# Optimization experiments

Hardware: AMD Instinct MI355X
Metric: run time of the kernel (lower is better)

The kernel has to match this reference:

```python
import jax, jax.numpy as jnp
import numpy as np

NUM_HEADS = 4
LN_EPS = 1e-5


def setup_inputs() -> dict:
    key = jax.random.key(0)
    ks = jax.random.split(key, 5)
    C = 256
    x = jax.random.normal(ks[0], (2, C, 64, 64), dtype=jnp.float32)
    in_proj_w = jax.random.normal(ks[1], (3 * C, C), dtype=jnp.float32) * (1.0 / np.sqrt(C))
    in_proj_b = jax.random.normal(ks[2], (3 * C,), dtype=jnp.float32) * 0.02
    out_w = jax.random.normal(ks[3], (C, C), dtype=jnp.float32) * (1.0 / np.sqrt(C))
    out_b = jax.random.normal(ks[4], (C,), dtype=jnp.float32) * 0.02
    ln_g = jnp.ones((C,), dtype=jnp.float32)
    ln_b = jnp.zeros((C,), dtype=jnp.float32)
    return {"x": x, "in_proj_w": in_proj_w, "in_proj_b": in_proj_b,
            "out_w": out_w, "out_b": out_b, "ln_g": ln_g, "ln_b": ln_b}


def reference(x, in_proj_w, in_proj_b, out_w, out_b, ln_g, ln_b):
    b, c, H, W = x.shape
    S = H * W  # 4096 == max_tokens -> no pooling, no interpolation
    hd = c // NUM_HEADS
    t = x.reshape(b, c, S).transpose(0, 2, 1)  # (b, S, c)
    # fused QKV projection (in_proj_weight is [3c, c], rows = q,k,v blocks)
    qkv = t @ in_proj_w.T + in_proj_b  # (b, S, 3c)
    q, k, v = jnp.split(qkv, 3, axis=-1)
    def to_heads(a):
        return a.reshape(b, S, NUM_HEADS, hd).transpose(0, 2, 1, 3)  # (b, h, S, d)
    q = to_heads(q) * (1.0 / np.sqrt(hd))
    k = to_heads(k)
    v = to_heads(v)
    scores = jnp.einsum('bhqd,bhkd->bhqk', q, k)      # (b, h, S, S)
    probs = jax.nn.softmax(scores, axis=-1)
    attn = jnp.einsum('bhqk,bhkd->bhqd', probs, v)    # (b, h, S, d)
    attn = attn.transpose(0, 2, 1, 3).reshape(b, S, c)
    out = attn @ out_w.T + out_b                      # output projection
    # LayerNorm over channel dim
    mu = jnp.mean(out, axis=-1, keepdims=True)
    var = jnp.mean(jnp.square(out - mu), axis=-1, keepdims=True)
    out = (out - mu) * jax.lax.rsqrt(var + LN_EPS) * ln_g + ln_b
    return out.transpose(0, 2, 1).reshape(b, c, H, W)
```

## Files before the change

kernel.cpp:

```cpp
#include <hip/hip_runtime.h>
#include <cstddef>

#define S_TOK 4096
#define CDIM 256
#define NHEADS 4
#define HDIM 64
#define LSK 72
#define LDA 36
#define LDY 264
#define LOG2E 1.44269504f

typedef __attribute__((ext_vector_type(8))) short short8;
typedef __attribute__((ext_vector_type(4))) float floatx4;

__device__ inline unsigned short f2bf(float f) {
  union { float f; unsigned u; } v;
  v.f = f;
  unsigned r = v.u + 0x7fff + ((v.u >> 16) & 1);
  return (unsigned short)(r >> 16);
}
__device__ inline float bf2f(unsigned short u) {
  union { unsigned u; float f; } v;
  v.u = ((unsigned)u) << 16;
  return v.f;
}
__device__ inline unsigned pack_bf16(float a, float b) {
#if __has_builtin(__builtin_amdgcn_cvt_pk_bf16_f32)
  typedef __bf16 bf16x2 __attribute__((ext_vector_type(2)));
  union { bf16x2 v; unsigned u; } r;
  r.v = __builtin_amdgcn_cvt_pk_bf16_f32(a, b);
  return r.u;
#else
  return ((unsigned)f2bf(b) << 16) | f2bf(a);
#endif
}

__global__ __launch_bounds__(256) void prep_kernel(
    const float* __restrict__ x, const float* __restrict__ ipw,
    const float* __restrict__ ow, unsigned short* __restrict__ wbf,
    unsigned short* __restrict__ owbf, unsigned short* __restrict__ xbfT) {
  __shared__ __align__(16) unsigned short T[64 * 72];
  const int tid = threadIdx.x;
  if (blockIdx.x < 256) {
    int idx = blockIdx.x * 256 + tid;
    float4 f;
    unsigned short* dst;
    if (idx < 49152) {
      f = ((const float4*)ipw)[idx];
      dst = wbf + idx * 4;
    } else {
      int j = idx - 49152;
      f = ((const float4*)ow)[j];
      dst = owbf + j * 4;
    }
    ushort4 u;
    u.x = f2bf(f.x); u.y = f2bf(f.y); u.z = f2bf(f.z); u.w = f2bf(f.w);
    *(ushort4*)dst = u;
    return;
  }
  const int bid = blockIdx.x - 256;
  const int s0 = (bid & 63) * 64, c0 = ((bid >> 6) & 3) * 64, b = bid >> 8;
  const int c_l = tid >> 2, q4 = tid & 3;
  const float4* src = (const float4*)(x + (((size_t)(b * CDIM + c0 + c_l)) << 12) + s0);
#pragma unroll
  for (int i = 0; i < 4; ++i) {
    int chunk = i * 4 + q4;
    float4 f = src[chunk];
    T[(chunk * 4 + 0) * 72 + c_l] = f2bf(f.x);
    T[(chunk * 4 + 1) * 72 + c_l] = f2bf(f.y);
    T[(chunk * 4 + 2) * 72 + c_l] = f2bf(f.z);
    T[(chunk * 4 + 3) * 72 + c_l] = f2bf(f.w);
  }
  __syncthreads();
  const int s_l = tid >> 2;
  unsigned short* drow = xbfT + ((size_t)((b << 12) + s0 + s_l)) * CDIM + c0;
#pragma unroll
  for (int i = 0; i < 2; ++i) {
    int chunk = i * 4 + q4;
    uint4 u = *(const uint4*)&T[s_l * 72 + chunk * 8];
    *(uint4*)(drow + chunk * 8) = u;
  }
}

__global__ __launch_bounds__(256) void qkv_gemm_kernel(
    const unsigned short* __restrict__ xbfT, const unsigned short* __restrict__ wbf,
    const float* __restrict__ ipb, unsigned short* __restrict__ q16,
    unsigned short* __restrict__ k16, unsigned short* __restrict__ vt16) {
  __shared__ __align__(16) unsigned short As[128 * LDA];
  __shared__ __align__(16) unsigned short Bs[64 * LDA];
  const int tid = threadIdx.x;
  const int wave = tid >> 6, lane = tid & 63;
  const int quad = lane >> 4, l16 = lane & 15;
  const int n0 = blockIdx.x * 64;
  const int tok0 = blockIdx.y * 128;
  const int b = blockIdx.z;

  const int r1 = tid >> 2, c1 = tid & 3;
  const unsigned short* gA = xbfT + ((size_t)(b * S_TOK + tok0 + r1)) * CDIM + c1 * 8;
  const unsigned short* gB = wbf + ((size_t)(n0 + r1)) * CDIM + c1 * 8;
  unsigned short* wA = &As[r1 * LDA + c1 * 8];
  unsigned short* wB = &Bs[r1 * LDA + c1 * 8];

  floatx4 acc[2][4];
#pragma unroll
  for (int mt = 0; mt < 2; ++mt)
#pragma unroll
    for (int nt = 0; nt < 4; ++nt) acc[mt][nt] = (floatx4){0.f, 0.f, 0.f, 0.f};

  uint4 a0p = *(const uint4*)(gA);
  uint4 a1p = *(const uint4*)(gA + 64 * CDIM);
  uint4 b0p = *(const uint4*)(gB);

  for (int ks = 0; ks < 8; ++ks) {
    __syncthreads();
    *(uint4*)wA = a0p;
    *(uint4*)(wA + 64 * LDA) = a1p;
    *(uint4*)wB = b0p;
    __syncthreads();
    if (ks < 7) {
      int off = (ks + 1) * 32;
      a0p = *(const uint4*)(gA + off);
      a1p = *(const uint4*)(gA + 64 * CDIM + off);
      b0p = *(const uint4*)(gB + off);
    }
    short8 af[2], bf[4];
#pragma unroll
    for (int mt = 0; mt < 2; ++mt)
      af[mt] = *(const short8*)&As[(wave * 32 + mt * 16 + l16) * LDA + quad * 8];
#pragma unroll
    for (int nt = 0; nt < 4; ++nt)
      bf[nt] = *(const short8*)&Bs[(nt * 16 + l16) * LDA + quad * 8];
#pragma unroll
    for (int mt = 0; mt < 2; ++mt)
#pragma unroll
      for (int nt = 0; nt < 4; ++nt)
        acc[mt][nt] = __builtin_amdgcn_mfma_f32_16x16x32_bf16(af[mt], bf[nt], acc[mt][nt], 0, 0, 0);
  }

  const int slab = n0 >> 8;
  int cb[4];
  float bias4[4];
#pragma unroll
  for (int nt = 0; nt < 4; ++nt) {
    cb[nt] = n0 + nt * 16 + l16;
    bias4[nt] = ipb[cb[nt]];
  }
  if (slab == 2) {
#pragma unroll
    for (int mt = 0; mt < 2; ++mt) {
      int tok = tok0 + wave * 32 + mt * 16 + quad * 4;
#pragma unroll
      for (int nt = 0; nt < 4; ++nt) {
        int dh = cb[nt] & 63, h = (cb[nt] >> 6) & 3;
        uint2 u;
        u.x = pack_bf16(acc[mt][nt][0] + bias4[nt], acc[mt][nt][1] + bias4[nt]);
        u.y = pack_bf16(acc[mt][nt][2] + bias4[nt], acc[mt][nt][3] + bias4[nt]);
        *(uint2*)&vt16[((size_t)((b * NHEADS + h) * HDIM + dh)) * S_TOK + tok] = u;
      }
    }
  } else {
    unsigned short* dst = slab ? k16 : q16;
    const float sc = slab ? 1.0f : 0.125f * LOG2E;
#pragma unroll
    for (int mt = 0; mt < 2; ++mt)
#pragma unroll
      for (int nt = 0; nt < 4; ++nt) {
        int dh = cb[nt] & 63, h = (cb[nt] >> 6) & 3;
        size_t base = ((size_t)(b * NHEADS + h) * S_TOK);
#pragma unroll
        for (int r = 0; r < 4; ++r) {
          int tok = tok0 + wave * 32 + mt * 16 + quad * 4 + r;
          dst[(base + tok) * HDIM + dh] = f2bf((acc[mt][nt][r] + bias4[nt]) * sc);
        }
      }
  }
}

__global__ __launch_bounds__(256) void attn_kernel(
    const unsigned short* __restrict__ q16,
    const unsigned short* __restrict__ k16,
    const unsigned short* __restrict__ vt16,
    unsigned short* __restrict__ op, float* __restrict__ lp) {
  __shared__ __align__(16) unsigned short Ks[64 * LSK];
  __shared__ __align__(16) unsigned short Vt[64 * LSK];
  __shared__ __align__(16) unsigned short Ps[4 * 64 * LSK];

  const int tid = threadIdx.x;
  const int wave = tid >> 6;
  const int lane = tid & 63;
  const int quad = lane >> 4;
  const int l16 = lane & 15;
  const int bh = blockIdx.y;
  const int q0 = blockIdx.x * 256;
  const int split = blockIdx.z;
  const int kt0 = split * 16;

  short8 qf[4][2];
#pragma unroll
  for (int mt = 0; mt < 4; ++mt) {
    const unsigned short* qg =
        q16 + ((size_t)bh * S_TOK + q0 + wave * 64 + mt * 16 + l16) * HDIM + quad * 8;
    qf[mt][0] = *(const short8*)(qg);
    qf[mt][1] = *(const short8*)(qg + 32);
  }

  const int sr = tid >> 3, scc = tid & 7;
  const unsigned short* kg = k16 + ((size_t)bh * S_TOK + sr) * HDIM + scc * 8;
  const unsigned short* vg = vt16 + ((size_t)bh * HDIM + sr) * S_TOK + scc * 8;
  unsigned short* ksw = &Ks[sr * LSK + scc * 8];
  unsigned short* vtw = &Vt[sr * LSK + scc * 8];

  floatx4 O[4][4];
  float lsum[4] = {0.f, 0.f, 0.f, 0.f};
#pragma unroll
  for (int mt = 0; mt < 4; ++mt)
#pragma unroll
    for (int nt = 0; nt < 4; ++nt) O[mt][nt] = (floatx4){0.f, 0.f, 0.f, 0.f};

  uint4 k0r = *(const uint4*)(kg + (size_t)kt0 * 64 * HDIM);
  uint4 k1r = *(const uint4*)(kg + (size_t)kt0 * 64 * HDIM + 32 * HDIM);
  uint4 v0r = *(const uint4*)(vg + kt0 * 64);
  uint4 v1r = *(const uint4*)(vg + kt0 * 64 + (size_t)32 * S_TOK);

  unsigned short* pw = &Ps[(wave * 64) * LSK];

  for (int t = 0; t < 16; ++t) {
    __syncthreads();
    *(uint4*)ksw = k0r;
    *(uint4*)(ksw + 32 * LSK) = k1r;
    *(uint4*)vtw = v0r;
    *(uint4*)(vtw + 32 * LSK) = v1r;
    __syncthreads();
    if (t < 15) {
      const unsigned short* kgn = kg + (size_t)(kt0 + t + 1) * 64 * HDIM;
      const unsigned short* vgn = vg + (kt0 + t + 1) * 64;
      k0r = *(const uint4*)(kgn);
      k1r = *(const uint4*)(kgn + 32 * HDIM);
      v0r = *(const uint4*)(vgn);
      v1r = *(const uint4*)(vgn + (size_t)32 * S_TOK);
    }

#pragma unroll
    for (int kt = 0; kt < 4; ++kt) {
      short8 kf0 = *(const short8*)(&Ks[(kt * 16 + l16) * LSK + quad * 8]);
      short8 kf1 = *(const short8*)(&Ks[(kt * 16 + l16) * LSK + 32 + quad * 8]);
#pragma unroll
      for (int mt = 0; mt < 4; ++mt) {
        floatx4 c = (floatx4){0.f, 0.f, 0.f, 0.f};
        c = __builtin_amdgcn_mfma_f32_16x16x32_bf16(kf0, qf[mt][0], c, 0, 0, 0);
        c = __builtin_amdgcn_mfma_f32_16x16x32_bf16(kf1, qf[mt][1], c, 0, 0, 0);
        float p0 = __builtin_amdgcn_exp2f(c[0]);
        float p1 = __builtin_amdgcn_exp2f(c[1]);
        float p2 = __builtin_amdgcn_exp2f(c[2]);
        float p3 = __builtin_amdgcn_exp2f(c[3]);
        lsum[mt] += (p0 + p1) + (p2 + p3);
        uint2 pk;
        pk.x = pack_bf16(p0, p1);
        pk.y = pack_bf16(p2, p3);
        *(uint2*)&pw[(mt * 16 + l16) * LSK + kt * 16 + quad * 4] = pk;
      }
    }

    short8 pf[4][2];
#pragma unroll
    for (int mt = 0; mt < 4; ++mt) {
      pf[mt][0] = *(const short8*)(&pw[(mt * 16 + l16) * LSK + quad * 8]);
      pf[mt][1] = *(const short8*)(&pw[(mt * 16 + l16) * LSK + 32 + quad * 8]);
    }
#pragma unroll
    for (int nt = 0; nt < 4; ++nt) {
      short8 vf0 = *(const short8*)(&Vt[(nt * 16 + l16) * LSK + quad * 8]);
      short8 vf1 = *(const short8*)(&Vt[(nt * 16 + l16) * LSK + 32 + quad * 8]);
#pragma unroll
      for (int mt = 0; mt < 4; ++mt) {
        O[mt][nt] = __builtin_amdgcn_mfma_f32_16x16x32_bf16(pf[mt][0], vf0, O[mt][nt], 0, 0, 0);
        O[mt][nt] = __builtin_amdgcn_mfma_f32_16x16x32_bf16(pf[mt][1], vf1, O[mt][nt], 0, 0, 0);
      }
    }
  }

  const int b = bh >> 2, h = bh & 3;
  unsigned short* op_s = op + (size_t)split * 2097152;
  float* lp_s = lp + (size_t)split * 32768;
#pragma unroll
  for (int mt = 0; mt < 4; ++mt) {
    float ls = lsum[mt];
    ls += __shfl_xor(ls, 16);
    ls += __shfl_xor(ls, 32);
    if (quad == 0)
      lp_s[bh * S_TOK + q0 + wave * 64 + mt * 16 + l16] = ls;
#pragma unroll
    for (int r = 0; r < 4; ++r) {
      int row = q0 + wave * 64 + mt * 16 + quad * 4 + r;
#pragma unroll
      for (int nt = 0; nt < 4; ++nt)
        op_s[((size_t)(b * S_TOK + row)) * CDIM + h * HDIM + nt * 16 + l16] =
            f2bf(O[mt][nt][r]);
    }
  }
}

__device__ inline unsigned merge2(const unsigned short* op, size_t off, float rinv) {
  float lo = 0.f, hi = 0.f;
#pragma unroll
  for (int sp = 0; sp < 4; ++sp) {
    unsigned u = *(const unsigned*)(op + (size_t)sp * 2097152 + off);
    lo += bf2f((unsigned short)(u & 0xffff));
    hi += bf2f((unsigned short)(u >> 16));
  }
  return pack_bf16(lo * rinv, hi * rinv);
}

__global__ __launch_bounds__(256) void out_ln_gemm_kernel(
    const unsigned short* __restrict__ op, const float* __restrict__ lp,
    const unsigned short* __restrict__ owbf, const float* __restrict__ obias,
    const float* __restrict__ lng, const float* __restrict__ lnb,
    float* __restrict__ out) {
  __shared__ __align__(16) unsigned short As[16 * LDA];
  __shared__ __align__(16) unsigned short Bs[256 * LDA];
  __shared__ __align__(16) float ys[16 * LDY];
  __shared__ float rsum[64];
  const int tid = threadIdx.x;
  const int wave = tid >> 6, lane = tid & 63;
  const int quad = lane >> 4, l16 = lane & 15;
  const int tok0 = blockIdx.x * 16;

  if (tid < 64) {
    int t = tid >> 2, h = tid & 3;
    int bb = tok0 >> 12;
    int idx = (bb * 4 + h) * 4096 + (tok0 & 4095) + t;
    rsum[t * 4 + h] =
        1.0f / (lp[idx] + lp[32768 + idx] + lp[65536 + idx] + lp[98304 + idx]);
  }
  __syncthreads();

  const int ar = tid >> 4, ac = tid & 15;
  const size_t abase = (size_t)(tok0 + ar) * CDIM + ac * 2;
  unsigned short* wAp = &As[ar * LDA + ac * 2];
  const int br = tid >> 2, bc = tid & 3;
  const unsigned short* gB = owbf + ((size_t)br) * CDIM + bc * 8;
  unsigned short* wBp = &Bs[br * LDA + bc * 8];

  floatx4 acc[4];
#pragma unroll
  for (int nt = 0; nt < 4; ++nt) acc[nt] = (floatx4){0.f, 0.f, 0.f, 0.f};

  unsigned ap = merge2(op, abase, rsum[ar * 4]);
  uint4 bp[4];
#pragma unroll
  for (int i = 0; i < 4; ++i) bp[i] = *(const uint4*)(gB + (size_t)i * 64 * CDIM);

  for (int ks = 0; ks < 8; ++ks) {
    __syncthreads();
    *(unsigned*)wAp = ap;
#pragma unroll
    for (int i = 0; i < 4; ++i) *(uint4*)(wBp + i * 64 * LDA) = bp[i];
    __syncthreads();
    if (ks < 7) {
      int off = (ks + 1) * 32;
      ap = merge2(op, abase + off, rsum[ar * 4 + ((ks + 1) >> 1)]);
#pragma unroll
      for (int i = 0; i < 4; ++i)
        bp[i] = *(const uint4*)(gB + (size_t)i * 64 * CDIM + off);
    }
    short8 af = *(const short8*)&As[l16 * LDA + quad * 8];
    short8 bf[4];
#pragma unroll
    for (int nt = 0; nt < 4; ++nt)
      bf[nt] = *(const short8*)&Bs[(wave * 64 + nt * 16 + l16) * LDA + quad * 8];
#pragma unroll
    for (int nt = 0; nt < 4; ++nt)
      acc[nt] = __builtin_amdgcn_mfma_f32_16x16x32_bf16(af, bf[nt], acc[nt], 0, 0, 0);
  }

#pragma unroll
  for (int nt = 0; nt < 4; ++nt) {
    int c = wave * 64 + nt * 16 + l16;
    float bo = obias[c];
#pragma unroll
    for (int r = 0; r < 4; ++r)
      ys[(quad * 4 + r) * LDY + c] = acc[nt][r] + bo;
  }
  __syncthreads();

  const int gtok = tid >> 4, lx = tid & 15;
  float sum = 0.f, ssq = 0.f;
#pragma unroll
  for (int i = 0; i < 16; ++i) {
    float v = ys[gtok * LDY + i * 16 + lx];
    sum += v;
    ssq += v * v;
  }
  sum += __shfl_xor(sum, 1); ssq += __shfl_xor(ssq, 1);
  sum += __shfl_xor(sum, 2); ssq += __shfl_xor(ssq, 2);
  sum += __shfl_xor(sum, 4); ssq += __shfl_xor(ssq, 4);
  sum += __shfl_xor(sum, 8); ssq += __shfl_xor(ssq, 8);
  float mu = sum * (1.f / 256.f);
  float var = ssq * (1.f / 256.f) - mu * mu;
  float rstd = rsqrtf(var + 1e-5f);
  const int b2 = tok0 >> 12;
  const int sl = (tok0 & 4095) + gtok;
#pragma unroll
  for (int i = 0; i < 16; ++i) {
    int c = i * 16 + lx;
    float v = ys[gtok * LDY + c];
    out[(((size_t)(b2 * CDIM + c)) << 12) + sl] = (v - mu) * rstd * lng[c] + lnb[c];
  }
}

extern "C" void kernel_launch(void* const* d_in, const int* in_sizes, int n_in,
                              void* d_out, int out_size, void* d_ws, size_t ws_size,
                              hipStream_t stream) {
  const float* x = (const float*)d_in[0];
  const float* ipw = (const float*)d_in[1];
  const float* ipb = (const float*)d_in[2];
  const float* ow = (const float*)d_in[3];
  const float* ob = (const float*)d_in[4];
  const float* lng = (const float*)d_in[5];
  const float* lnb = (const float*)d_in[6];
  float* out = (float*)d_out;
  unsigned short* wbf = (unsigned short*)d_ws;
  unsigned short* owbf = wbf + 196608;
  unsigned short* xbfT = owbf + 65536;
  unsigned short* q16 = xbfT + 2097152;
  unsigned short* k16 = q16 + 2097152;
  unsigned short* vt16 = k16 + 2097152;
  unsigned short* op = vt16 + 2097152;
  float* lp = (float*)(op + 8388608);

  prep_kernel<<<768, 256, 0, stream>>>(x, ipw, ow, wbf, owbf, xbfT);
  qkv_gemm_kernel<<<dim3(12, 32, 2), 256, 0, stream>>>(xbfT, wbf, ipb, q16, k16, vt16);
  attn_kernel<<<dim3(16, 8, 4), 256, 0, stream>>>(q16, k16, vt16, op, lp);
  out_ln_gemm_kernel<<<512, 256, 0, stream>>>(op, lp, owbf, ob, lng, lnb, out);
}
```

Baseline: 168.1 us.

## Fuse fp32-to-bf16 prep into QKV and output GEMMs, retile both GEMMs

Removes the separate prep kernel. The QKV GEMM now reads fp32 x directly, transposing and converting it into shared memory, and converts the weight slices on the fly. Each block computes the matching Q, K and V columns for 64 tokens, so one A tile is reused across all three projections. The output GEMM converts the fp32 out-projection weights per block and doubles its token tile to 32, with a wider merge of the four partial attention outputs. This saves a kernel launch and the bf16 intermediate round trip. The cost is redundant weight conversion and larger fp32 weight reads in every block.

```diff
diff --git a/kernel.cpp b/kernel.cpp
--- a/kernel.cpp
+++ b/kernel.cpp
@@ -35,144 +35,106 @@
 #endif
 }
 
-__global__ __launch_bounds__(256) void prep_kernel(
+__global__ __launch_bounds__(256) void qkv_gemm_kernel(
     const float* __restrict__ x, const float* __restrict__ ipw,
-    const float* __restrict__ ow, unsigned short* __restrict__ wbf,
-    unsigned short* __restrict__ owbf, unsigned short* __restrict__ xbfT) {
-  __shared__ __align__(16) unsigned short T[64 * 72];
-  const int tid = threadIdx.x;
-  if (blockIdx.x < 256) {
-    int idx = blockIdx.x * 256 + tid;
-    float4 f;
-    unsigned short* dst;
-    if (idx < 49152) {
-      f = ((const float4*)ipw)[idx];
-      dst = wbf + idx * 4;
-    } else {
-      int j = idx - 49152;
-      f = ((const float4*)ow)[j];
-      dst = owbf + j * 4;
-    }
-    ushort4 u;
-    u.x = f2bf(f.x); u.y = f2bf(f.y); u.z = f2bf(f.z); u.w = f2bf(f.w);
-    *(ushort4*)dst = u;
-    return;
-  }
-  const int bid = blockIdx.x - 256;
-  const int s0 = (bid & 63) * 64, c0 = ((bid >> 6) & 3) * 64, b = bid >> 8;
-  const int c_l = tid >> 2, q4 = tid & 3;
-  const float4* src = (const float4*)(x + (((size_t)(b * CDIM + c0 + c_l)) << 12) + s0);
-#pragma unroll
-  for (int i = 0; i < 4; ++i) {
-    int chunk = i * 4 + q4;
-    float4 f = src[chunk];
-    T[(chunk * 4 + 0) * 72 + c_l] = f2bf(f.x);
-    T[(chunk * 4 + 1) * 72 + c_l] = f2bf(f.y);
-    T[(chunk * 4 + 2) * 72 + c_l] = f2bf(f.z);
-    T[(chunk * 4 + 3) * 72 + c_l] = f2bf(f.w);
-  }
-  __syncthreads();
-  const int s_l = tid >> 2;
-  unsigned short* drow = xbfT + ((size_t)((b << 12) + s0 + s_l)) * CDIM + c0;
-#pragma unroll
-  for (int i = 0; i < 2; ++i) {
-    int chunk = i * 4 + q4;
-    uint4 u = *(const uint4*)&T[s_l * 72 + chunk * 8];
-    *(uint4*)(drow + chunk * 8) = u;
-  }
-}
-
-__global__ __launch_bounds__(256) void qkv_gemm_kernel(
-    const unsigned short* __restrict__ xbfT, const unsigned short* __restrict__ wbf,
     const float* __restrict__ ipb, unsigned short* __restrict__ q16,
     unsigned short* __restrict__ k16, unsigned short* __restrict__ vt16) {
-  __shared__ __align__(16) unsigned short As[128 * LDA];
-  __shared__ __align__(16) unsigned short Bs[64 * LDA];
+  __shared__ __align__(16) unsigned short As[64 * LDA];
+  __shared__ __align__(16) unsigned short Bs[3][64 * LDA];
   const int tid = threadIdx.x;
   const int wave = tid >> 6, lane = tid & 63;
   const int quad = lane >> 4, l16 = lane & 15;
   const int n0 = blockIdx.x * 64;
-  const int tok0 = blockIdx.y * 128;
+  const int tok0 = blockIdx.y * 64;
   const int b = blockIdx.z;
 
-  const int r1 = tid >> 2, c1 = tid & 3;
-  const unsigned short* gA = xbfT + ((size_t)(b * S_TOK + tok0 + r1)) * CDIM + c1 * 8;
-  const unsigned short* gB = wbf + ((size_t)(n0 + r1)) * CDIM + c1 * 8;
-  unsigned short* wA = &As[r1 * LDA + c1 * 8];
-  unsigned short* wB = &Bs[r1 * LDA + c1 * 8];
-
-  floatx4 acc[2][4];
-#pragma unroll
-  for (int mt = 0; mt < 2; ++mt)
-#pragma unroll
-    for (int nt = 0; nt < 4; ++nt) acc[mt][nt] = (floatx4){0.f, 0.f, 0.f, 0.f};
-
-  uint4 a0p = *(const uint4*)(gA);
-  uint4 a1p = *(const uint4*)(gA + 64 * CDIM);
-  uint4 b0p = *(const uint4*)(gB);
+  const int c_l = tid >> 3, t8 = tid & 7;
+  const float* gx = x + (((size_t)(b * CDIM + c_l)) << 12) + tok0 + t8 * 8;
+  unsigned short* wa = &As[(t8 * 8) * LDA + c_l];
+
+  const int rr = tid >> 2, c4 = tid & 3;
+  const float* gw0 = ipw + ((size_t)(n0 + rr)) * CDIM + c4 * 8;
+  unsigned short* wb0 = &Bs[0][rr * LDA + c4 * 8];
+
+  floatx4 acc[3][4];
+#pragma unroll
+  for (int s = 0; s < 3; ++s)
+#pragma unroll
+    for (int nt = 0; nt < 4; ++nt) acc[s][nt] = (floatx4){0.f, 0.f, 0.f, 0.f};
+
+  float4 a0 = *(const float4*)(gx);
+  float4 a1 = *(const float4*)(gx + 4);
+  float4 bp[3][2];
+#pragma unroll
+  for (int s = 0; s < 3; ++s) {
+    bp[s][0] = *(const float4*)(gw0 + (size_t)s * 256 * CDIM);
+    bp[s][1] = *(const float4*)(gw0 + (size_t)s * 256 * CDIM + 4);
+  }
 
   for (int ks = 0; ks < 8; ++ks) {
     __syncthreads();
-    *(uint4*)wA = a0p;
-    *(uint4*)(wA + 64 * LDA) = a1p;
-    *(uint4*)wB = b0p;
+    {
+      unsigned p;
+      p = pack_bf16(a0.x, a0.y);
+      wa[0 * LDA] = (unsigned short)p; wa[1 * LDA] = (unsigned short)(p >> 16);
+      p = pack_bf16(a0.z, a0.w);
+      wa[2 * LDA] = (unsigned short)p; wa[3 * LDA] = (unsigned short)(p >> 16);
+      p = pack_bf16(a1.x, a1.y);
+      wa[4 * LDA] = (unsigned short)p; wa[5 * LDA] = (unsigned short)(p >> 16);
+      p = pack_bf16(a1.z, a1.w);
+      wa[6 * LDA] = (unsigned short)p; wa[7 * LDA] = (unsigned short)(p >> 16);
+    }
+#pragma unroll
+    for (int s = 0; s < 3; ++s) {
+      uint2 u0, u1;
+      u0.x = pack_bf16(bp[s][0].x, bp[s][0].y);
+      u0.y = pack_bf16(bp[s][0].z, bp[s][0].w);
+      u1.x = pack_bf16(bp[s][1].x, bp[s][1].y);
+      u1.y = pack_bf16(bp[s][1].z, bp[s][1].w);
+      unsigned short* w = wb0 + s * 64 * LDA;
+      *(uint2*)w = u0;
+      *(uint2*)(w + 4) = u1;
+    }
     __syncthreads();
     if (ks < 7) {
-      int off = (ks + 1) * 32;
-      a0p = *(const uint4*)(gA + off);
-      a1p = *(const uint4*)(gA + 64 * CDIM + off);
-      b0p = *(const uint4*)(gB + off);
-    }
-    short8 af[2], bf[4];
-#pragma unroll
-    for (int mt = 0; mt < 2; ++mt)
-      af[mt] = *(const short8*)&As[(wave * 32 + mt * 16 + l16) * LDA + quad * 8];
-#pragma unroll
-    for (int nt = 0; nt < 4; ++nt)
-      bf[nt] = *(const short8*)&Bs[(nt * 16 + l16) * LDA + quad * 8];
-#pragma unroll
-    for (int mt = 0; mt < 2; ++mt)
-#pragma unroll
-      for (int nt = 0; nt < 4; ++nt)
-        acc[mt][nt] = __builtin_amdgcn_mfma_f32_16x16x32_bf16(af[mt], bf[nt], acc[mt][nt], 0, 0, 0);
-  }
-
-  const int slab = n0 >> 8;
-  int cb[4];
-  float bias4[4];
+      const float* gxn = gx + ((size_t)((ks + 1) * 32) << 12);
+      a0 = *(const float4*)(gxn);
+      a1 = *(const float4*)(gxn + 4);
+#pragma unroll
+      for (int s = 0; s < 3; ++s) {
+        const float* g = gw0 + (size_t)s * 256 * CDIM + (ks + 1) * 32;
+        bp[s][0] = *(const float4*)(g);
+        bp[s][1] = *(const float4*)(g + 4);
+      }
+    }
+    short8 af = *(const short8*)&As[(wave * 16 + l16) * LDA + quad * 8];
+#pragma unroll
+    for (int s = 0; s < 3; ++s)
+#pragma unroll
+      for (int nt = 0; nt < 4; ++nt) {
+        short8 bf = *(const short8*)&Bs[s][(nt * 16 + l16) * LDA + quad * 8];
+        acc[s][nt] = __builtin_amdgcn_mfma_f32_16x16x32_bf16(af, bf, acc[s][nt], 0, 0, 0);
+      }
+  }
+
+  const float qsc = 0.125f * LOG2E;
 #pragma unroll
   for (int nt = 0; nt < 4; ++nt) {
-    cb[nt] = n0 + nt * 16 + l16;
-    bias4[nt] = ipb[cb[nt]];
-  }
-  if (slab == 2) {
-#pragma unroll
-    for (int mt = 0; mt < 2; ++mt) {
-      int tok = tok0 + wave * 32 + mt * 16 + quad * 4;
-#pragma unroll
-      for (int nt = 0; nt < 4; ++nt) {
-        int dh = cb[nt] & 63, h = (cb[nt] >> 6) & 3;
-        uint2 u;
-        u.x = pack_bf16(acc[mt][nt][0] + bias4[nt], acc[mt][nt][1] + bias4[nt]);
-        u.y = pack_bf16(acc[mt][nt][2] + bias4[nt], acc[mt][nt][3] + bias4[nt]);
-        *(uint2*)&vt16[((size_t)((b * NHEADS + h) * HDIM + dh)) * S_TOK + tok] = u;
-      }
-    }
-  } else {
-    unsigned short* dst = slab ? k16 : q16;
-    const float sc = slab ? 1.0f : 0.125f * LOG2E;
-#pragma unroll
-    for (int mt = 0; mt < 2; ++mt)
-#pragma unroll
-      for (int nt = 0; nt < 4; ++nt) {
-        int dh = cb[nt] & 63, h = (cb[nt] >> 6) & 3;
-        size_t base = ((size_t)(b * NHEADS + h) * S_TOK);
-#pragma unroll
-        for (int r = 0; r < 4; ++r) {
-          int tok = tok0 + wave * 32 + mt * 16 + quad * 4 + r;
-          dst[(base + tok) * HDIM + dh] = f2bf((acc[mt][nt][r] + bias4[nt]) * sc);
-        }
-      }
+    int cb = n0 + nt * 16 + l16;
+    int h = cb >> 6, dh = cb & 63;
+    float bq = ipb[cb], bk = ipb[256 + cb], bv = ipb[512 + cb];
+    size_t base = ((size_t)(b * NHEADS + h)) * S_TOK;
+#pragma unroll
+    for (int r = 0; r < 4; ++r) {
+      int tok = tok0 + wave * 16 + quad * 4 + r;
+      q16[(base + tok) * HDIM + dh] = f2bf((acc[0][nt][r] + bq) * qsc);
+      k16[(base + tok) * HDIM + dh] = f2bf(acc[1][nt][r] + bk);
+    }
+    int tokv = tok0 + wave * 16 + quad * 4;
+    uint2 u;
+    u.x = pack_bf16(acc[2][nt][0] + bv, acc[2][nt][1] + bv);
+    u.y = pack_bf16(acc[2][nt][2] + bv, acc[2][nt][3] + bv);
+    *(uint2*)&vt16[(base * 0 + ((size_t)(b * NHEADS + h) * HDIM + dh)) * S_TOK + tokv] = u;
   }
 }
 
@@ -300,109 +262,136 @@
   }
 }
 
-__device__ inline unsigned merge2(const unsigned short* op, size_t off, float rinv) {
-  float lo = 0.f, hi = 0.f;
+__device__ inline uint2 merge4(const unsigned short* op, size_t off, float rinv) {
+  float s0 = 0.f, s1 = 0.f, s2 = 0.f, s3 = 0.f;
 #pragma unroll
   for (int sp = 0; sp < 4; ++sp) {
-    unsigned u = *(const unsigned*)(op + (size_t)sp * 2097152 + off);
-    lo += bf2f((unsigned short)(u & 0xffff));
-    hi += bf2f((unsigned short)(u >> 16));
-  }
-  return pack_bf16(lo * rinv, hi * rinv);
+    uint2 u = *(const uint2*)(op + (size_t)sp * 2097152 + off);
+    s0 += bf2f((unsigned short)(u.x & 0xffff));
+    s1 += bf2f((unsigned short)(u.x >> 16));
+    s2 += bf2f((unsigned short)(u.y & 0xffff));
+    s3 += bf2f((unsigned short)(u.y >> 16));
+  }
+  uint2 r;
+  r.x = pack_bf16(s0 * rinv, s1 * rinv);
+  r.y = pack_bf16(s2 * rinv, s3 * rinv);
+  return r;
 }
 
 __global__ __launch_bounds__(256) void out_ln_gemm_kernel(
     const unsigned short* __restrict__ op, const float* __restrict__ lp,
-    const unsigned short* __restrict__ owbf, const float* __restrict__ obias,
+    const float* __restrict__ ow, const float* __restrict__ obias,
     const float* __restrict__ lng, const float* __restrict__ lnb,
     float* __restrict__ out) {
-  __shared__ __align__(16) unsigned short As[16 * LDA];
+  __shared__ __align__(16) unsigned short As[32 * LDA];
   __shared__ __align__(16) unsigned short Bs[256 * LDA];
-  __shared__ __align__(16) float ys[16 * LDY];
-  __shared__ float rsum[64];
+  __shared__ __align__(16) float ys[32 * LDY];
+  __shared__ float rsum[128];
   const int tid = threadIdx.x;
   const int wave = tid >> 6, lane = tid & 63;
   const int quad = lane >> 4, l16 = lane & 15;
-  const int tok0 = blockIdx.x * 16;
-
-  if (tid < 64) {
+  const int tok0 = blockIdx.x * 32;
+
+  if (tid < 128) {
     int t = tid >> 2, h = tid & 3;
     int bb = tok0 >> 12;
     int idx = (bb * 4 + h) * 4096 + (tok0 & 4095) + t;
-    rsum[t * 4 + h] =
+    rsum[tid] =
         1.0f / (lp[idx] + lp[32768 + idx] + lp[65536 + idx] + lp[98304 + idx]);
   }
   __syncthreads();
 
-  const int ar = tid >> 4, ac = tid & 15;
-  const size_t abase = (size_t)(tok0 + ar) * CDIM + ac * 2;
-  unsigned short* wAp = &As[ar * LDA + ac * 2];
-  const int br = tid >> 2, bc = tid & 3;
-  const unsigned short* gB = owbf + ((size_t)br) * CDIM + bc * 8;
-  unsigned short* wBp = &Bs[br * LDA + bc * 8];
-
-  floatx4 acc[4];
-#pragma unroll
-  for (int nt = 0; nt < 4; ++nt) acc[nt] = (floatx4){0.f, 0.f, 0.f, 0.f};
-
-  unsigned ap = merge2(op, abase, rsum[ar * 4]);
-  uint4 bp[4];
-#pragma unroll
-  for (int i = 0; i < 4; ++i) bp[i] = *(const uint4*)(gB + (size_t)i * 64 * CDIM);
+  const int ar = tid >> 3, ac = tid & 7;
+  const size_t abase = (size_t)(tok0 + ar) * CDIM + ac * 4;
+  unsigned short* wAp = &As[ar * LDA + ac * 4];
+  const int rr = tid >> 2, c4 = tid & 3;
+  const float* gB = ow + (size_t)rr * CDIM + c4 * 8;
+  unsigned short* wBp = &Bs[rr * LDA + c4 * 8];
+
+  floatx4 acc[2][4];
+#pragma unroll
+  for (int mt = 0; mt < 2; ++mt)
+#pragma unroll
+    for (int nt = 0; nt < 4; ++nt) acc[mt][nt] = (floatx4){0.f, 0.f, 0.f, 0.f};
+
+  uint2 ap = merge4(op, abase, rsum[(ar << 2) + (ac >> 4)]);
+  float4 bpf[4][2];
+#pragma unroll
+  for (int i = 0; i < 4; ++i) {
+    bpf[i][0] = *(const float4*)(gB + (size_t)i * 64 * CDIM);
+    bpf[i][1] = *(const float4*)(gB + (size_t)i * 64 * CDIM + 4);
+  }
 
   for (int ks = 0; ks < 8; ++ks) {
     __syncthreads();
-    *(unsigned*)wAp = ap;
-#pragma unroll
-    for (int i = 0; i < 4; ++i) *(uint4*)(wBp + i * 64 * LDA) = bp[i];
+    *(uint2*)wAp = ap;
+#pragma unroll
+    for (int i = 0; i < 4; ++i) {
+      uint2 u0, u1;
+      u0.x = pack_bf16(bpf[i][0].x, bpf[i][0].y);
+      u0.y = pack_bf16(bpf[i][0].z, bpf[i][0].w);
+      u1.x = pack_bf16(bpf[i][1].x, bpf[i][1].y);
+      u1.y = pack_bf16(bpf[i][1].z, bpf[i][1].w);
+      unsigned short* w = wBp + i * 64 * LDA;
+      *(uint2*)w = u0;
+      *(uint2*)(w + 4) = u1;
+    }
     __syncthreads();
     if (ks < 7) {
       int off = (ks + 1) * 32;
-      ap = merge2(op, abase + off, rsum[ar * 4 + ((ks + 1) >> 1)]);
-#pragma unroll
-      for (int i = 0; i < 4; ++i)
-        bp[i] = *(const uint4*)(gB + (size_t)i * 64 * CDIM + off);
-    }
-    short8 af = *(const short8*)&As[l16 * LDA + quad * 8];
-    short8 bf[4];
+      int ch = off + ac * 4;
+      ap = merge4(op, abase + off, rsum[(ar << 2) + (ch >> 6)]);
+#pragma unroll
+      for (int i = 0; i < 4; ++i) {
+        bpf[i][0] = *(const float4*)(gB + (size_t)i * 64 * CDIM + off);
+        bpf[i][1] = *(const float4*)(gB + (size_t)i * 64 * CDIM + off + 4);
+      }
+    }
+    short8 af[2], bf[4];
+#pragma unroll
+    for (int mt = 0; mt < 2; ++mt)
+      af[mt] = *(const short8*)&As[(mt * 16 + l16) * LDA + quad * 8];
 #pragma unroll
     for (int nt = 0; nt < 4; ++nt)
       bf[nt] = *(const short8*)&Bs[(wave * 64 + nt * 16 + l16) * LDA + quad * 8];
 #pragma unroll
-    for (int nt = 0; nt < 4; ++nt)
-      acc[nt] = __builtin_amdgcn_mfma_f32_16x16x32_bf16(af, bf[nt], acc[nt], 0, 0, 0);
-  }
-
-#pragma unroll
-  for (int nt = 0; nt < 4; ++nt) {
-    int c = wave * 64 + nt * 16 + l16;
-    float bo = obias[c];
-#pragma unroll
-    for (int r = 0; r < 4; ++r)
-      ys[(quad * 4 + r) * LDY + c] = acc[nt][r] + bo;
-  }
+    for (int mt = 0; mt < 2; ++mt)
+#pragma unroll
+      for (int nt = 0; nt < 4; ++nt)
+        acc[mt][nt] = __builtin_amdgcn_mfma_f32_16x16x32_bf16(af[mt], bf[nt], acc[mt][nt], 0, 0, 0);
+  }
+
+#pragma unroll
+  for (int mt = 0; mt < 2; ++mt)
+#pragma unroll
+    for (int nt = 0; nt < 4; ++nt) {
+      int c = wave * 64 + nt * 16 + l16;
+      float bo = obias[c];
+#pragma unroll
+      for (int r = 0; r < 4; ++r)
+        ys[(mt * 16 + quad * 4 + r) * LDY + c] = acc[mt][nt][r] + bo;
+    }
   __syncthreads();
 
-  const int gtok = tid >> 4, lx = tid & 15;
+  const int gtok = tid >> 3, l8 = tid & 7;
   float sum = 0.f, ssq = 0.f;
 #pragma unroll
-  for (int i = 0; i < 16; ++i) {
-    float v = ys[gtok * LDY + i * 16 + lx];
+  for (int i = 0; i < 32; ++i) {
+    float v = ys[gtok * LDY + i * 8 + l8];
     sum += v;
     ssq += v * v;
   }
   sum += __shfl_xor(sum, 1); ssq += __shfl_xor(ssq, 1);
   sum += __shfl_xor(sum, 2); ssq += __shfl_xor(ssq, 2);
   sum += __shfl_xor(sum, 4); ssq += __shfl_xor(ssq, 4);
-  sum += __shfl_xor(sum, 8); ssq += __shfl_xor(ssq, 8);
   float mu = sum * (1.f / 256.f);
   float var = ssq * (1.f / 256.f) - mu * mu;
   float rstd = rsqrtf(var + 1e-5f);
   const int b2 = tok0 >> 12;
   const int sl = (tok0 & 4095) + gtok;
 #pragma unroll
-  for (int i = 0; i < 16; ++i) {
-    int c = i * 16 + lx;
+  for (int i = 0; i < 32; ++i) {
+    int c = i * 8 + l8;
     float v = ys[gtok * LDY + c];
     out[(((size_t)(b2 * CDIM + c)) << 12) + sl] = (v - mu) * rstd * lng[c] + lnb[c];
   }
@@ -419,17 +408,13 @@
   const float* lng = (const float*)d_in[5];
   const float* lnb = (const float*)d_in[6];
   float* out = (float*)d_out;
-  unsigned short* wbf = (unsigned short*)d_ws;
-  unsigned short* owbf = wbf + 196608;
-  unsigned short* xbfT = owbf + 65536;
-  unsigned short* q16 = xbfT + 2097152;
+  unsigned short* q16 = (unsigned short*)d_ws;
   unsigned short* k16 = q16 + 2097152;
   unsigned short* vt16 = k16 + 2097152;
   unsigned short* op = vt16 + 2097152;
   float* lp = (float*)(op + 8388608);
 
-  prep_kernel<<<768, 256, 0, stream>>>(x, ipw, ow, wbf, owbf, xbfT);
-  qkv_gemm_kernel<<<dim3(12, 32, 2), 256, 0, stream>>>(xbfT, wbf, ipb, q16, k16, vt16);
+  qkv_gemm_kernel<<<dim3(4, 64, 2), 256, 0, stream>>>(x, ipw, ipb, q16, k16, vt16);
   attn_kernel<<<dim3(16, 8, 4), 256, 0, stream>>>(q16, k16, vt16, op, lp);
-  out_ln_gemm_kernel<<<512, 256, 0, stream>>>(op, lp, owbf, ob, lng, lnb, out);
-}
+  out_ln_gemm_kernel<<<256, 256, 0, stream>>>(op, lp, ow, ob, lng, lnb, out);
+}
```

Measured after the change: 149.6 us. -11.0%, faster.
